# Kernel tuning notes

Measured on AMD Instinct MI355X. Metric: run time of the kernel, lower is better.

## Reference

```python
import jax, jax.numpy as jnp
import numpy as np

# Static graph layout: B equal-sized graphs so per-graph k is constant (jit-friendly).
NUM_GRAPHS = 128
NODES_PER_GRAPH = 1024
NUM_NODES = NUM_GRAPHS * NODES_PER_GRAPH  # 131072
NUM_EDGES = NUM_NODES * 32               # 4194304
CHANNELS = 256
RATIO = 0.5
K = max(1, int(NODES_PER_GRAPH * RATIO))  # 512, matches max(1, int(count*ratio))


def setup_inputs() -> dict:
    key = jax.random.key(0)
    k0, k1, k2, k3 = jax.random.split(key, 4)
    x = jax.random.normal(k0, (NUM_NODES, CHANNELS), dtype=jnp.float32)
    edge_index = jax.random.randint(k1, (2, NUM_EDGES), 0, NUM_NODES, dtype=jnp.int64)
    batch = (jnp.arange(NUM_NODES, dtype=jnp.int64) // NODES_PER_GRAPH)
    # score MLP params: Linear(C, C) -> tanh -> Linear(C, 1)
    s = 1.0 / np.sqrt(CHANNELS)
    W1 = jax.random.uniform(k2, (CHANNELS, CHANNELS), jnp.float32, -s, s)
    b1 = jnp.zeros((CHANNELS,), jnp.float32)
    W2 = jax.random.uniform(k3, (CHANNELS, 1), jnp.float32, -s, s)
    b2 = jnp.zeros((1,), jnp.float32)
    return {"x": x, "edge_index": edge_index, "batch": batch,
            "W1": W1, "b1": b1, "W2": W2, "b2": b2}


def reference(x, edge_index, batch, W1, b1, W2, b2):
    # Note: SAGPool.forward computes a GNN score then discards it and calls
    # super().forward, which recomputes scores with the self.score MLP. The GNN
    # path is dead code (and would error in torch); the effective math is below.
    scores = (jnp.tanh(x @ W1 + b1) @ W2 + b2)[:, 0]  # [num_nodes]

    # Per-graph top-k, vectorized across all graphs (equal-sized segments).
    s = scores.reshape(NUM_GRAPHS, NODES_PER_GRAPH)
    top_s, top_i = jax.lax.top_k(s, K)  # descending per graph, matches torch.topk
    offsets = (jnp.arange(NUM_GRAPHS, dtype=top_i.dtype) * NODES_PER_GRAPH)[:, None]
    perm = (top_i + offsets).reshape(-1)  # [B*K] global indices, graphs in order

    x_pooled = x[perm]
    batch_pooled = batch[perm]
    scores_pooled = top_s.reshape(-1)

    # Edge filtering: keep edges whose both endpoints survive.
    keep = jnp.zeros((NUM_NODES,), dtype=bool).at[perm].set(True)
    row, col = edge_index
    edge_mask = keep[row] & keep[col]
    # Static-shape compaction: stable-sort kept edges to the front, pad with -1.
    order = jnp.argsort(~edge_mask, stable=True)
    edge_index_pooled = jnp.where(edge_mask[order][None, :], edge_index[:, order], -1)

    return x_pooled, edge_index_pooled, batch_pooled, perm, scores_pooled
```

## Files before the change

kernel.cpp:

```cpp
#include <hip/hip_runtime.h>
#include <hip/hip_bf16.h>

#define NG 128
#define NPG 1024
#define NN (NG * NPG)
#define NE (NN * 32)
#define CH 256
#define KSEL 512

#define CAP 128
#define EPS 0.02f

#define OUT_X      0
#define OUT_EDGE   16777216
#define OUT_BATCH  25165824
#define OUT_PERM   25231360
#define OUT_SCORES 25296896

#define WS_SCORES  0
#define WS_KEEP    524288
#define WS_COUNTS  540672
#define WS_OFFSETS 544768
#define WS_BFRAG   548864
#define WS_BIDX    679936
#define WS_BSCORE  745472
#define WS_BN      811008
#define WS_BLO     811520

typedef __attribute__((ext_vector_type(8))) short bf16x8;
typedef __attribute__((ext_vector_type(4))) float f32x4;

__device__ __forceinline__ unsigned short f2bf(float f) {
    unsigned int b = __float_as_uint(f);
    return (unsigned short)((b + 0x7fffu + ((b >> 16) & 1u)) >> 16);
}

__device__ __forceinline__ unsigned int cvt2bf(float lo, float hi) {
    union { __hip_bfloat162 h; unsigned int u; } c;
    c.h = __float22bfloat162_rn(make_float2(lo, hi));
    return c.u;
}

__device__ __forceinline__ float tanh_fast(float h) {
    const float e = __expf(2.0f * h);
    return 1.0f - 2.0f / (e + 1.0f);
}

__global__ __launch_bounds__(256)
void k_cvtW(const float* __restrict__ W1, unsigned short* __restrict__ W1b,
            unsigned int* __restrict__ keep_bits)
{
    const int t = blockIdx.x * 256 + threadIdx.x;
    if (t < NN / 32) keep_bits[t] = 0u;
    const int s    = t >> 10;
    const int rem  = t & 1023;
    const int n    = rem >> 6;
    const int lane = rem & 63;
    const int kbase = s * 32 + (lane >> 4) * 8;
    const int col   = n * 16 + (lane & 15);
    unsigned short u[8];
    #pragma unroll
    for (int j = 0; j < 8; ++j)
        u[j] = f2bf(W1[(size_t)(kbase + j) * CH + col]);
    uint4 v;
    v.x = u[0] | ((unsigned int)u[1] << 16);
    v.y = u[2] | ((unsigned int)u[3] << 16);
    v.z = u[4] | ((unsigned int)u[5] << 16);
    v.w = u[6] | ((unsigned int)u[7] << 16);
    *(uint4*)&W1b[(size_t)t * 8] = v;
}

__global__ __launch_bounds__(256, 4)
void k_mfma_scores(const float* __restrict__ x, const unsigned short* __restrict__ W1b,
                   const float* __restrict__ b1, const float* __restrict__ W2,
                   const float* __restrict__ b2, float* __restrict__ scores)
{
    __shared__ __align__(16) short As[64 * 256];
    __shared__ float epi[4][64];

    const int tid = threadIdx.x;
    const int w_  = tid >> 6;
    const int l   = tid & 63;
    const int n0  = blockIdx.x * 64;

    #pragma unroll
    for (int it = 0; it < 16; ++it) {
        const int flat = it * 1024 + tid * 4;
        const int row = flat >> 8;
        const int c   = flat & 255;
        const float4 v = *(const float4*)&x[(size_t)(n0 + row) * CH + c];
        uint2 p;
        p.x = cvt2bf(v.x, v.y);
        p.y = cvt2bf(v.z, v.w);
        const int byte = (row * 512 + c * 2) ^ ((row & 7) << 4);
        *(uint2*)((char*)As + byte) = p;
    }
    __syncthreads();

    f32x4 acc[4][4];
    #pragma unroll
    for (int m = 0; m < 4; ++m)
        #pragma unroll
        for (int n = 0; n < 4; ++n)
            acc[m][n] = (f32x4){0.f, 0.f, 0.f, 0.f};

    const unsigned short* Wl = W1b + l * 8;
    bf16x8 bc[4], bn[4];
    #pragma unroll
    for (int ni = 0; ni < 4; ++ni)
        bc[ni] = *(const bf16x8*)&Wl[(size_t)(w_ * 4 + ni) * 512];

    #pragma unroll
    for (int s = 0; s < 8; ++s) {
        if (s < 7) {
            #pragma unroll
            for (int ni = 0; ni < 4; ++ni)
                bn[ni] = *(const bf16x8*)&Wl[(size_t)((s + 1) * 16 + w_ * 4 + ni) * 512];
        }
        bf16x8 a[4];
        #pragma unroll
        for (int m = 0; m < 4; ++m) {
            const int row  = m * 16 + (l & 15);
            const int byte = (row * 512 + s * 64 + ((l >> 4) * 16)) ^ ((l & 7) << 4);
            a[m] = *(const bf16x8*)((const char*)As + byte);
        }
        #pragma unroll
        for (int ni = 0; ni < 4; ++ni)
            #pragma unroll
            for (int m = 0; m < 4; ++m)
                acc[m][ni] = __builtin_amdgcn_mfma_f32_16x16x32_bf16(a[m], bc[ni], acc[m][ni], 0, 0, 0);
        #pragma unroll
        for (int ni = 0; ni < 4; ++ni) bc[ni] = bn[ni];
    }

    float part[16];
    #pragma unroll
    for (int i = 0; i < 16; ++i) part[i] = 0.f;
    #pragma unroll
    for (int ni = 0; ni < 4; ++ni) {
        const int col = w_ * 64 + ni * 16 + (l & 15);
        const float b1c = b1[col];
        const float w2c = W2[col];
        #pragma unroll
        for (int m = 0; m < 4; ++m)
            #pragma unroll
            for (int r = 0; r < 4; ++r)
                part[m * 4 + r] += tanh_fast(acc[m][ni][r] + b1c) * w2c;
    }
    #pragma unroll
    for (int off = 1; off < 16; off <<= 1)
        #pragma unroll
        for (int i = 0; i < 16; ++i)
            part[i] += __shfl_xor(part[i], off, 64);

    if ((l & 15) == 0) {
        const int gq = l >> 4;
        #pragma unroll
        for (int m = 0; m < 4; ++m)
            #pragma unroll
            for (int r = 0; r < 4; ++r)
                epi[w_][m * 16 + gq * 4 + r] = part[m * 4 + r];
    }
    __syncthreads();
    if (tid < 64)
        scores[n0 + tid] = epi[0][tid] + epi[1][tid] + epi[2][tid] + epi[3][tid] + b2[0];
}

__global__ __launch_bounds__(256)
void k_topk(const float* __restrict__ scores, float* __restrict__ out,
            unsigned int* __restrict__ keep_bits, int* __restrict__ band_idx,
            int* __restrict__ band_n, int* __restrict__ band_lo)
{
    __shared__ float    sf[1024];
    __shared__ unsigned uk[1024];
    __shared__ int      hist[256];
    __shared__ int      cge[256];
    __shared__ unsigned s_prefix;
    __shared__ int      s_rank;
    __shared__ int      wtot[4];

    const int g = blockIdx.x;
    const int t = threadIdx.x;

    #pragma unroll
    for (int h = 0; h < 4; ++h) {
        const int i = h * 256 + t;
        const float f = scores[g * NPG + i];
        sf[i] = f;
        const unsigned b = __float_as_uint(f);
        uk[i] = (b & 0x80000000u) ? ~b : (b | 0x80000000u);
    }
    if (t == 0) { s_prefix = 0u; s_rank = KSEL; }
    __syncthreads();

    const unsigned pmaskv[4] = {0u, 0xFF000000u, 0xFFFF0000u, 0xFFFFFF00u};
    #pragma unroll
    for (int pass = 0; pass < 4; ++pass) {
        const int shift = 24 - pass * 8;
        hist[t] = 0;
        __syncthreads();
        const unsigned pm  = pmaskv[pass];
        const unsigned pfx = s_prefix;
        #pragma unroll
        for (int h = 0; h < 4; ++h) {
            const unsigned u = uk[h * 256 + t];
            if ((u & pm) == pfx) atomicAdd(&hist[(u >> shift) & 255], 1);
        }
        __syncthreads();
        cge[t] = hist[t];
        __syncthreads();
        #pragma unroll
        for (int off = 1; off < 256; off <<= 1) {
            const int v = (t + off < 256) ? cge[t + off] : 0;
            __syncthreads();
            cge[t] += v;
            __syncthreads();
        }
        const int r = s_rank;
        const int above = (t == 255) ? 0 : cge[t + 1];
        if (cge[t] >= r && above < r) {
            s_prefix = pfx | ((unsigned)t << shift);
            s_rank   = r - above;
        }
        __syncthreads();
    }

    const unsigned u512 = s_prefix;
    const unsigned fb = (u512 & 0x80000000u) ? (u512 & 0x7FFFFFFFu) : ~u512;
    const float tau = __uint_as_float(fb);

    bool cert[4], bnd[4];
    int myc = 0, myb = 0;
    #pragma unroll
    for (int j = 0; j < 4; ++j) {
        const float f = sf[t * 4 + j];
        cert[j] = (f > tau + EPS);
        bnd[j]  = (!cert[j]) && (f >= tau - EPS);
        myc += cert[j] ? 1 : 0;
        myb += bnd[j] ? 1 : 0;
    }
    const int pack = (myc << 16) | myb;
    const int lane = t & 63, w = t >> 6;
    int incl = pack;
    #pragma unroll
    for (int off = 1; off < 64; off <<= 1) {
        const int v = __shfl_up(incl, off, 64);
        if (lane >= off) incl += v;
    }
    if (lane == 63) wtot[w] = incl;
    __syncthreads();
    int wbase = 0;
    for (int i = 0; i < w; ++i) wbase += wtot[i];
    const int excl = wbase + incl - pack;
    int cpos = excl >> 16;
    int bpos = excl & 0xFFFF;
    const int total = wtot[0] + wtot[1] + wtot[2] + wtot[3];

    #pragma unroll
    for (int j = 0; j < 4; ++j) {
        const int li = t * 4 + j;
        if (cert[j]) {
            const int gi = g * NPG + li;
            out[OUT_PERM   + g * KSEL + cpos] = (float)gi;
            out[OUT_SCORES + g * KSEL + cpos] = sf[li];
            atomicOr(&keep_bits[gi >> 5], 1u << (gi & 31));
            ++cpos;
        } else if (bnd[j]) {
            if (bpos < CAP) band_idx[g * CAP + bpos] = li;
            ++bpos;
        }
    }
    out[OUT_BATCH + g * KSEL + t]       = (float)g;
    out[OUT_BATCH + g * KSEL + t + 256] = (float)g;
    if (t == 0) {
        band_lo[g] = (total >> 16);
        band_n[g]  = min(total & 0xFFFF, CAP);
    }
}

__global__ __launch_bounds__(256, 2)
void k_rescore(const float* __restrict__ x, const float* __restrict__ W1,
               const float* __restrict__ b1, const float* __restrict__ W2,
               const float* __restrict__ b2, const int* __restrict__ band_idx,
               const int* __restrict__ band_n, float* __restrict__ band_scores)
{
    const int g = blockIdx.x >> 2;
    const int c0 = (blockIdx.x & 3) * 32;
    if (band_n[g] <= c0) return;

    __shared__ __align__(16) float W1s[16][CH];
    __shared__ __align__(16) float Xs[32][16];

    const int tid = threadIdx.x;
    const int w_  = tid >> 6;
    const int l   = tid & 63;

    int iv = 0;
    if (w_ < 2) iv = band_idx[g * CAP + c0 + w_ * 16 + (l >> 2)] & 1023;
    const float* xg = x + ((size_t)g * NPG + iv) * CH;

    const float4 b1v = *(const float4*)&b1[l * 4];
    float acc[8][4];
    #pragma unroll
    for (int n = 0; n < 8; ++n) {
        acc[n][0] = b1v.x; acc[n][1] = b1v.y; acc[n][2] = b1v.z; acc[n][3] = b1v.w;
    }

    for (int kc = 0; kc < 16; ++kc) {
        __syncthreads();
        #pragma unroll
        for (int it = 0; it < 4; ++it) {
            const float* gp = W1 + (size_t)kc * (16 * CH) + (w_ * 4 + it) * CH + l * 4;
            float* lb = &W1s[0][0] + (w_ * 4 + it) * CH;
            __builtin_amdgcn_global_load_lds(
                (const __attribute__((address_space(1))) void*)gp,
                (__attribute__((address_space(3))) void*)lb, 16, 0, 0);
        }
        if (w_ < 2) {
            const float* gp = xg + kc * 16 + (l & 3) * 4;
            float* lb = &Xs[0][0] + w_ * 256;
            __builtin_amdgcn_global_load_lds(
                (const __attribute__((address_space(1))) void*)gp,
                (__attribute__((address_space(3))) void*)lb, 16, 0, 0);
        }
        __syncthreads();

        #pragma unroll
        for (int kq = 0; kq < 4; ++kq) {
            const int k4 = kq * 4;
            const float4 wv0 = *(const float4*)&W1s[k4 + 0][l * 4];
            const float4 wv1 = *(const float4*)&W1s[k4 + 1][l * 4];
            const float4 wv2 = *(const float4*)&W1s[k4 + 2][l * 4];
            const float4 wv3 = *(const float4*)&W1s[k4 + 3][l * 4];
            #pragma unroll
            for (int n = 0; n < 8; ++n) {
                const float4 xv = *(const float4*)&Xs[w_ * 8 + n][k4];
                acc[n][0] = fmaf(xv.x, wv0.x, acc[n][0]);
                acc[n][1] = fmaf(xv.x, wv0.y, acc[n][1]);
                acc[n][2] = fmaf(xv.x, wv0.z, acc[n][2]);
                acc[n][3] = fmaf(xv.x, wv0.w, acc[n][3]);
                acc[n][0] = fmaf(xv.y, wv1.x, acc[n][0]);
                acc[n][1] = fmaf(xv.y, wv1.y, acc[n][1]);
                acc[n][2] = fmaf(xv.y, wv1.z, acc[n][2]);
                acc[n][3] = fmaf(xv.y, wv1.w, acc[n][3]);
                acc[n][0] = fmaf(xv.z, wv2.x, acc[n][0]);
                acc[n][1] = fmaf(xv.z, wv2.y, acc[n][1]);
                acc[n][2] = fmaf(xv.z, wv2.z, acc[n][2]);
                acc[n][3] = fmaf(xv.z, wv2.w, acc[n][3]);
                acc[n][0] = fmaf(xv.w, wv3.x, acc[n][0]);
                acc[n][1] = fmaf(xv.w, wv3.y, acc[n][1]);
                acc[n][2] = fmaf(xv.w, wv3.z, acc[n][2]);
                acc[n][3] = fmaf(xv.w, wv3.w, acc[n][3]);
            }
        }
    }

    const float4 w2v = *(const float4*)&W2[l * 4];
    const float  bb  = b2[0];
    float s_[8];
    #pragma unroll
    for (int n = 0; n < 8; ++n) {
        s_[n] = tanhf(acc[n][0]) * w2v.x + tanhf(acc[n][1]) * w2v.y
              + tanhf(acc[n][2]) * w2v.z + tanhf(acc[n][3]) * w2v.w;
    }
    #pragma unroll
    for (int off = 1; off < 64; off <<= 1)
        #pragma unroll
        for (int n = 0; n < 8; ++n)
            s_[n] += __shfl_xor(s_[n], off, 64);

    if (l == 0) {
        #pragma unroll
        for (int n = 0; n < 8; ++n)
            band_scores[g * CAP + c0 + w_ * 8 + n] = s_[n] + bb;
    }
}

__global__ __launch_bounds__(64)
void k_bandsel(const float* __restrict__ band_scores, const int* __restrict__ band_idx,
               const int* __restrict__ band_n, const int* __restrict__ band_lo,
               float* __restrict__ out, unsigned int* __restrict__ keep_bits)
{
    __shared__ float bs[CAP];
    __shared__ int   bi[CAP];
    const int g = blockIdx.x;
    const int t = threadIdx.x;
    const int n  = band_n[g];
    const int lo = band_lo[g];
    int needed = KSEL - lo;
    if (needed > n) needed = n;

    #pragma unroll
    for (int h = 0; h < 2; ++h) {
        const int q = t + h * 64;
        const bool valid = q < n;
        bs[q] = valid ? band_scores[g * CAP + q] : -3.402823466e+38f;
        bi[q] = valid ? band_idx[g * CAP + q] : (NPG + q);
    }
    __syncthreads();
    for (int size = 2; size <= CAP; size <<= 1) {
        for (int stride = size >> 1; stride > 0; stride >>= 1) {
            __syncthreads();
            const int lo_i = ((t & ~(stride - 1)) << 1) | (t & (stride - 1));
            const int hi_i = lo_i + stride;
            const bool dirDesc = ((lo_i & size) == 0);
            const float va = bs[lo_i], vb = bs[hi_i];
            const int ia = bi[lo_i], ib = bi[hi_i];
            const bool aB = (va > vb) || (va == vb && ia < ib);
            if (aB != dirDesc) {
                bs[lo_i] = vb; bs[hi_i] = va;
                bi[lo_i] = ib; bi[hi_i] = ia;
            }
        }
    }
    __syncthreads();
    #pragma unroll
    for (int h = 0; h < 2; ++h) {
        const int s = t + h * 64;
        if (s < needed) {
            const int li = bi[s];
            const int gi = g * NPG + li;
            out[OUT_PERM   + g * KSEL + lo + s] = (float)gi;
            out[OUT_SCORES + g * KSEL + lo + s] = bs[s];
            atomicOr(&keep_bits[gi >> 5], 1u << (gi & 31));
        }
    }
}

__global__ __launch_bounds__(256)
void k_gather(const float* __restrict__ x, const float* __restrict__ perm_f,
              float* __restrict__ out_x)
{
    const int row  = blockIdx.x * 4 + (threadIdx.x >> 6);
    const int lane = threadIdx.x & 63;
    const int pi = (int)perm_f[row];
    const float4* src = (const float4*)&x[(size_t)pi * CH];
    float4* dst = (float4*)&out_x[(size_t)row * CH];
    dst[lane] = src[lane];
}

__global__ __launch_bounds__(256)
void k_edgecount(const int* __restrict__ ei, const unsigned int* __restrict__ keep_bits,
                 int* __restrict__ counts, float* __restrict__ out_edge)
{
    const int t = threadIdx.x;
    const float4 neg = make_float4(-1.f, -1.f, -1.f, -1.f);
    #pragma unroll
    for (int q = 0; q < 4; ++q) {
        ((float4*)out_edge)[(size_t)blockIdx.x * 1024 + q * 256 + t] = neg;
        ((float4*)(out_edge + NE))[(size_t)blockIdx.x * 1024 + q * 256 + t] = neg;
    }

    const size_t base = (size_t)blockIdx.x * 4096 + (size_t)t * 16;
    const int* rowp = ei;
    const int* colp = ei + NE;
    int rv[16], cv[16];
    #pragma unroll
    for (int q = 0; q < 4; ++q) {
        int4 r4 = *(const int4*)&rowp[base + q * 4];
        int4 c4 = *(const int4*)&colp[base + q * 4];
        rv[q*4+0]=r4.x; rv[q*4+1]=r4.y; rv[q*4+2]=r4.z; rv[q*4+3]=r4.w;
        cv[q*4+0]=c4.x; cv[q*4+1]=c4.y; cv[q*4+2]=c4.z; cv[q*4+3]=c4.w;
    }
    int cnt = 0;
    #pragma unroll
    for (int q = 0; q < 16; ++q)
        cnt += (int)((keep_bits[rv[q] >> 5] >> (rv[q] & 31)) &
                     (keep_bits[cv[q] >> 5] >> (cv[q] & 31)) & 1u);

    #pragma unroll
    for (int off = 1; off < 64; off <<= 1) cnt += __shfl_xor(cnt, off, 64);
    __shared__ int wsum[4];
    if ((t & 63) == 0) wsum[t >> 6] = cnt;
    __syncthreads();
    if (t == 0) counts[blockIdx.x] = wsum[0] + wsum[1] + wsum[2] + wsum[3];
}

__global__ __launch_bounds__(1024)
void k_scan(const int* __restrict__ counts, int* __restrict__ offsets)
{
    __shared__ int tmp[1024];
    const int t = threadIdx.x;
    const int c = counts[t];
    tmp[t] = c;
    __syncthreads();
    for (int off = 1; off < 1024; off <<= 1) {
        int v = (t >= off) ? tmp[t - off] : 0;
        __syncthreads();
        tmp[t] += v;
        __syncthreads();
    }
    offsets[t] = tmp[t] - c;
}

__global__ __launch_bounds__(256)
void k_scatter(const int* __restrict__ ei, const unsigned int* __restrict__ keep_bits,
               const int* __restrict__ offsets, float* __restrict__ out_edge)
{
    const int t = threadIdx.x;
    const size_t base = (size_t)blockIdx.x * 4096 + (size_t)t * 16;
    const int* rowp = ei;
    const int* colp = ei + NE;
    int rv[16], cv[16];
    #pragma unroll
    for (int q = 0; q < 4; ++q) {
        int4 r4 = *(const int4*)&rowp[base + q * 4];
        int4 c4 = *(const int4*)&colp[base + q * 4];
        rv[q*4+0]=r4.x; rv[q*4+1]=r4.y; rv[q*4+2]=r4.z; rv[q*4+3]=r4.w;
        cv[q*4+0]=c4.x; cv[q*4+1]=c4.y; cv[q*4+2]=c4.z; cv[q*4+3]=c4.w;
    }
    unsigned m = 0; int cnt = 0;
    #pragma unroll
    for (int q = 0; q < 16; ++q) {
        const bool kk = ((keep_bits[rv[q] >> 5] >> (rv[q] & 31)) &
                         (keep_bits[cv[q] >> 5] >> (cv[q] & 31)) & 1u) != 0u;
        m |= ((unsigned)kk) << q;
        cnt += (int)kk;
    }
    const int lane = t & 63, w = t >> 6;
    int incl = cnt;
    #pragma unroll
    for (int off = 1; off < 64; off <<= 1) {
        int v = __shfl_up(incl, off, 64);
        if (lane >= off) incl += v;
    }
    __shared__ int wtot[4];
    if (lane == 63) wtot[w] = incl;
    __syncthreads();
    int wbase = 0;
    for (int i = 0; i < w; ++i) wbase += wtot[i];
    int pos = offsets[blockIdx.x] + wbase + (incl - cnt);
    #pragma unroll
    for (int q = 0; q < 16; ++q) {
        if (m & (1u << q)) {
            out_edge[pos]      = (float)rv[q];
            out_edge[NE + pos] = (float)cv[q];
            ++pos;
        }
    }
}

extern "C" void kernel_launch(void* const* d_in, const int* in_sizes, int n_in,
                              void* d_out, int out_size, void* d_ws, size_t ws_size,
                              hipStream_t stream)
{
    const float* x  = (const float*)d_in[0];
    const int*   ei = (const int*)d_in[1];
    const float* W1 = (const float*)d_in[3];
    const float* b1 = (const float*)d_in[4];
    const float* W2 = (const float*)d_in[5];
    const float* b2 = (const float*)d_in[6];

    float* out = (float*)d_out;
    char*  ws  = (char*)d_ws;
    float*          scores    = (float*)(ws + WS_SCORES);
    unsigned int*   keep_bits = (unsigned int*)(ws + WS_KEEP);
    int*            counts    = (int*)(ws + WS_COUNTS);
    int*            offsets   = (int*)(ws + WS_OFFSETS);
    unsigned short* W1b       = (unsigned short*)(ws + WS_BFRAG);
    int*            band_idx  = (int*)(ws + WS_BIDX);
    float*          band_sc   = (float*)(ws + WS_BSCORE);
    int*            band_n    = (int*)(ws + WS_BN);
    int*            band_lo   = (int*)(ws + WS_BLO);

    k_cvtW<<<32, 256, 0, stream>>>(W1, W1b, keep_bits);
    k_mfma_scores<<<NN / 64, 256, 0, stream>>>(x, W1b, b1, W2, b2, scores);
    k_topk<<<NG, 256, 0, stream>>>(scores, out, keep_bits, band_idx, band_n, band_lo);
    k_rescore<<<NG * (CAP / 32), 256, 0, stream>>>(x, W1, b1, W2, b2, band_idx, band_n, band_sc);
    k_bandsel<<<NG, 64, 0, stream>>>(band_sc, band_idx, band_n, band_lo, out, keep_bits);
    k_gather<<<(NG * KSEL) / 4, 256, 0, stream>>>(x, out + OUT_PERM, out + OUT_X);
    k_edgecount<<<NE / 4096, 256, 0, stream>>>(ei, keep_bits, counts, out + OUT_EDGE);
    k_scan<<<1, 1024, 0, stream>>>(counts, offsets);
    k_scatter<<<NE / 4096, 256, 0, stream>>>(ei, keep_bits, offsets, out + OUT_EDGE);
}
```

Before: 158.7 us.

## Fuse row gather into topk/bandsel and fold block scan into scatter

Removes the standalone gather kernel by having k_topk copy the certain rows (via a shared-memory slot map) and k_bandsel copy the band-selected rows directly. Removes the single-block scan kernel by having each scatter block sum all preceding block counts itself. This cuts two launches and the perm read-back. The cost is that only 128 blocks do the gather, the bandsel copy is a serial loop in one 64-thread block, and the scatter prefix is redundant O(blocks) work per block.

```diff
diff --git a/kernel.cpp b/kernel.cpp
--- a/kernel.cpp
+++ b/kernel.cpp
@@ -167,9 +167,9 @@
 }
 
 __global__ __launch_bounds__(256)
-void k_topk(const float* __restrict__ scores, float* __restrict__ out,
-            unsigned int* __restrict__ keep_bits, int* __restrict__ band_idx,
-            int* __restrict__ band_n, int* __restrict__ band_lo)
+void k_topk(const float* __restrict__ scores, const float* __restrict__ x,
+            float* __restrict__ out, unsigned int* __restrict__ keep_bits,
+            int* __restrict__ band_idx, int* __restrict__ band_n, int* __restrict__ band_lo)
 {
     __shared__ float    sf[1024];
     __shared__ unsigned uk[1024];
@@ -255,7 +255,9 @@
     int cpos = excl >> 16;
     int bpos = excl & 0xFFFF;
     const int total = wtot[0] + wtot[1] + wtot[2] + wtot[3];
-
+    const int lo_cnt = total >> 16;
+
+    int* cmap = (int*)uk;
     #pragma unroll
     for (int j = 0; j < 4; ++j) {
         const int li = t * 4 + j;
@@ -263,6 +265,7 @@
             const int gi = g * NPG + li;
             out[OUT_PERM   + g * KSEL + cpos] = (float)gi;
             out[OUT_SCORES + g * KSEL + cpos] = sf[li];
+            cmap[cpos] = li;
             atomicOr(&keep_bits[gi >> 5], 1u << (gi & 31));
             ++cpos;
         } else if (bnd[j]) {
@@ -273,8 +276,16 @@
     out[OUT_BATCH + g * KSEL + t]       = (float)g;
     out[OUT_BATCH + g * KSEL + t + 256] = (float)g;
     if (t == 0) {
-        band_lo[g] = (total >> 16);
+        band_lo[g] = lo_cnt;
         band_n[g]  = min(total & 0xFFFF, CAP);
+    }
+    __syncthreads();
+
+    for (int slot = w; slot < lo_cnt; slot += 4) {
+        const int li = cmap[slot];
+        const float4* src = (const float4*)&x[((size_t)g * NPG + li) * CH];
+        float4* dst = (float4*)&out[OUT_X + (size_t)(g * KSEL + slot) * CH];
+        dst[lane] = src[lane];
     }
 }
 
@@ -379,7 +390,8 @@
 __global__ __launch_bounds__(64)
 void k_bandsel(const float* __restrict__ band_scores, const int* __restrict__ band_idx,
                const int* __restrict__ band_n, const int* __restrict__ band_lo,
-               float* __restrict__ out, unsigned int* __restrict__ keep_bits)
+               const float* __restrict__ x, float* __restrict__ out,
+               unsigned int* __restrict__ keep_bits)
 {
     __shared__ float bs[CAP];
     __shared__ int   bi[CAP];
@@ -425,18 +437,12 @@
             atomicOr(&keep_bits[gi >> 5], 1u << (gi & 31));
         }
     }
-}
-
-__global__ __launch_bounds__(256)
-void k_gather(const float* __restrict__ x, const float* __restrict__ perm_f,
-              float* __restrict__ out_x)
-{
-    const int row  = blockIdx.x * 4 + (threadIdx.x >> 6);
-    const int lane = threadIdx.x & 63;
-    const int pi = (int)perm_f[row];
-    const float4* src = (const float4*)&x[(size_t)pi * CH];
-    float4* dst = (float4*)&out_x[(size_t)row * CH];
-    dst[lane] = src[lane];
+    for (int s = 0; s < needed; ++s) {
+        const int li = bi[s] & 1023;
+        const float4* src = (const float4*)&x[((size_t)g * NPG + li) * CH];
+        float4* dst = (float4*)&out[OUT_X + (size_t)(g * KSEL + lo + s) * CH];
+        dst[t] = src[t];
+    }
 }
 
 __global__ __launch_bounds__(256)
@@ -476,28 +482,20 @@
     if (t == 0) counts[blockIdx.x] = wsum[0] + wsum[1] + wsum[2] + wsum[3];
 }
 
-__global__ __launch_bounds__(1024)
-void k_scan(const int* __restrict__ counts, int* __restrict__ offsets)
-{
-    __shared__ int tmp[1024];
-    const int t = threadIdx.x;
-    const int c = counts[t];
-    tmp[t] = c;
-    __syncthreads();
-    for (int off = 1; off < 1024; off <<= 1) {
-        int v = (t >= off) ? tmp[t - off] : 0;
-        __syncthreads();
-        tmp[t] += v;
-        __syncthreads();
-    }
-    offsets[t] = tmp[t] - c;
-}
-
 __global__ __launch_bounds__(256)
 void k_scatter(const int* __restrict__ ei, const unsigned int* __restrict__ keep_bits,
-               const int* __restrict__ offsets, float* __restrict__ out_edge)
+               const int* __restrict__ counts, float* __restrict__ out_edge)
 {
     const int t = threadIdx.x;
+    const int lane = t & 63, w = t >> 6;
+
+    int pre = 0;
+    for (int i = t; i < blockIdx.x; i += 256) pre += counts[i];
+    #pragma unroll
+    for (int off = 1; off < 64; off <<= 1) pre += __shfl_xor(pre, off, 64);
+    __shared__ int wpre[4];
+    if (lane == 0) wpre[w] = pre;
+
     const size_t base = (size_t)blockIdx.x * 4096 + (size_t)t * 16;
     const int* rowp = ei;
     const int* colp = ei + NE;
@@ -517,7 +515,6 @@
         m |= ((unsigned)kk) << q;
         cnt += (int)kk;
     }
-    const int lane = t & 63, w = t >> 6;
     int incl = cnt;
     #pragma unroll
     for (int off = 1; off < 64; off <<= 1) {
@@ -527,9 +524,10 @@
     __shared__ int wtot[4];
     if (lane == 63) wtot[w] = incl;
     __syncthreads();
+    const int blk_base = wpre[0] + wpre[1] + wpre[2] + wpre[3];
     int wbase = 0;
     for (int i = 0; i < w; ++i) wbase += wtot[i];
-    int pos = offsets[blockIdx.x] + wbase + (incl - cnt);
+    int pos = blk_base + wbase + (incl - cnt);
     #pragma unroll
     for (int q = 0; q < 16; ++q) {
         if (m & (1u << q)) {
@@ -556,7 +554,6 @@
     float*          scores    = (float*)(ws + WS_SCORES);
     unsigned int*   keep_bits = (unsigned int*)(ws + WS_KEEP);
     int*            counts    = (int*)(ws + WS_COUNTS);
-    int*            offsets   = (int*)(ws + WS_OFFSETS);
     unsigned short* W1b       = (unsigned short*)(ws + WS_BFRAG);
     int*            band_idx  = (int*)(ws + WS_BIDX);
     float*          band_sc   = (float*)(ws + WS_BSCORE);
@@ -565,11 +562,9 @@
 
     k_cvtW<<<32, 256, 0, stream>>>(W1, W1b, keep_bits);
     k_mfma_scores<<<NN / 64, 256, 0, stream>>>(x, W1b, b1, W2, b2, scores);
-    k_topk<<<NG, 256, 0, stream>>>(scores, out, keep_bits, band_idx, band_n, band_lo);
+    k_topk<<<NG, 256, 0, stream>>>(scores, x, out, keep_bits, band_idx, band_n, band_lo);
     k_rescore<<<NG * (CAP / 32), 256, 0, stream>>>(x, W1, b1, W2, b2, band_idx, band_n, band_sc);
-    k_bandsel<<<NG, 64, 0, stream>>>(band_sc, band_idx, band_n, band_lo, out, keep_bits);
-    k_gather<<<(NG * KSEL) / 4, 256, 0, stream>>>(x, out + OUT_PERM, out + OUT_X);
+    k_bandsel<<<NG, 64, 0, stream>>>(band_sc, band_idx, band_n, band_lo, x, out, keep_bits);
     k_edgecount<<<NE / 4096, 256, 0, stream>>>(ei, keep_bits, counts, out + OUT_EDGE);
-    k_scan<<<1, 1024, 0, stream>>>(counts, offsets);
-    k_scatter<<<NE / 4096, 256, 0, stream>>>(ei, keep_bits, offsets, out + OUT_EDGE);
-}
+    k_scatter<<<NE / 4096, 256, 0, stream>>>(ei, keep_bits, counts, out + OUT_EDGE);
+}
```

Result: slower. 177.9 us (+12.1%).
